# Performance work log

Hardware: AMD Instinct MI355X
Metric: run time of the kernel (lower is better)

## Reference

```python
import jax, jax.numpy as jnp
import numpy as np
from jax import lax

IN_CH = 256
UP = 8
DN = ('NCHW', 'OIHW', 'NCHW')


def setup_inputs() -> dict:
    key = jax.random.key(0)
    ks = jax.random.split(key, 6)
    B, H, W = 8, 96, 96
    flow_lr = jax.random.normal(ks[0], (B, 2, H, W), dtype=jnp.float32)
    feat = jax.random.normal(ks[1], (B, IN_CH, H, W), dtype=jnp.float32)
    w1 = jax.random.normal(ks[2], (IN_CH, IN_CH, 3, 3), dtype=jnp.float32) * 0.02
    b1 = jnp.zeros((IN_CH,), dtype=jnp.float32)
    w2 = jax.random.normal(ks[3], (UP * UP * 9, IN_CH, 1, 1), dtype=jnp.float32) * 0.02
    b2 = jnp.zeros((UP * UP * 9,), dtype=jnp.float32)
    return {"flow_lr": flow_lr, "feat": feat, "w1": w1, "b1": b1, "w2": w2, "b2": b2}


def reference(flow_lr, feat, w1, b1, w2, b2):
    B, _, H, W = flow_lr.shape
    up = UP
    # mask head: 3x3 conv + relu + 1x1 conv
    x = lax.conv_general_dilated(feat, w1, (1, 1), 'SAME', dimension_numbers=DN)
    x = jax.nn.relu(x + b1[None, :, None, None])
    mask = lax.conv_general_dilated(x, w2, (1, 1), 'SAME', dimension_numbers=DN)
    mask = mask + b2[None, :, None, None]
    # channel dim 9*up*up splits as (9, up, up), matching torch .view(B,1,9,up,up,H,W)
    mask = mask.reshape(B, 9, up, up, H, W)
    mask = jax.nn.softmax(mask, axis=1)
    # unfold(flow_lr, 3, padding=1): 9 zero-padded 3x3 shifts, row-major (kh, kw)
    pad = jnp.pad(flow_lr, ((0, 0), (0, 0), (1, 1), (1, 1)))
    flow_unf = jnp.stack(
        [pad[:, :, i:i + H, j:j + W] for i in range(3) for j in range(3)], axis=2
    )  # (B, 2, 9, H, W)
    # convex combination over the 9 neighbors
    up_flow = jnp.einsum('bkpqhw,bckhw->bcpqhw', mask, flow_unf)  # (B,2,up,up,H,W)
    # pixel-shuffle: (B,2,p,q,H,W) -> (B,2,H,p,W,q) -> (B,2,H*up,W*up)
    up_flow = up_flow.transpose(0, 1, 4, 2, 5, 3).reshape(B, 2, H * up, W * up)
    return up_flow * up
```

## Files before the change

kernel.cpp:

```cpp
#include <hip/hip_runtime.h>
#include <hip/hip_bf16.h>
#include <stdint.h>

typedef unsigned short u16;
typedef __bf16 bf16x8 __attribute__((ext_vector_type(8)));
typedef float f32x4 __attribute__((ext_vector_type(4)));

#define MFMA16(a, b, c) __builtin_amdgcn_mfma_f32_16x16x32_bf16((a), (b), (c), 0, 0, 0)

#define GLOAD16(g, l)                                                        \
  __builtin_amdgcn_global_load_lds(                                          \
      (const __attribute__((address_space(1))) void*)(g),                    \
      (__attribute__((address_space(3))) void*)(l), 16, 0, 0)

static __device__ __forceinline__ u16 f2bf(float f) {
  union { float f; uint32_t u; } v;
  v.f = f;
  uint32_t u = v.u;
  return (u16)((u + 0x7FFFu + ((u >> 16) & 1u)) >> 16);
}
static __device__ __forceinline__ float u2f(uint32_t u) {
  union { uint32_t u; float f; } v;
  v.u = u;
  return v.f;
}

#define FEATT_ELEMS (8u * 98u * 98u * 256u)
#define W1T_OFF     FEATT_ELEMS
#define W1T_ELEMS   (256u * 2304u)
#define W2B_OFF     (W1T_OFF + W1T_ELEMS)
#define W2B_ELEMS   (576u * 256u)
#define X_OFF       (W2B_OFF + W2B_ELEMS)

__global__ __launch_bounds__(256) void halo_zero(u16* __restrict__ featT) {
  int tid = blockIdx.x * 256 + threadIdx.x;
  int b = tid / (388 * 32);
  int rem = tid % (388 * 32);
  int pos = rem >> 5, v = rem & 31;
  int h, w;
  if (pos < 98) { h = 0; w = pos; }
  else if (pos < 196) { h = 97; w = pos - 98; }
  else if (pos < 292) { h = pos - 196 + 1; w = 0; }
  else { h = pos - 292 + 1; w = 97; }
  uint4* dst = (uint4*)(featT + (size_t)((b * 98 + h) * 98 + w) * 256 + v * 8);
  *dst = make_uint4(0, 0, 0, 0);
}

__global__ __launch_bounds__(256) void prep_featT(const float* __restrict__ feat,
                                                  u16* __restrict__ featT) {
  const int pt = blockIdx.x, ct = blockIdx.y, b = blockIdx.z;
  const int p0 = pt * 64, c0 = ct * 64;
  __shared__ float tile[64][65];
  const int t = threadIdx.x;
  const int pj = t & 63, ci0 = t >> 6;
#pragma unroll
  for (int r = 0; r < 16; ++r) {
    int ci = r * 4 + ci0;
    tile[ci][pj] = feat[(b * 256 + c0 + ci) * 9216 + p0 + pj];
  }
  __syncthreads();
  const int pl = t >> 2, cc0 = (t & 3) * 16;
  const int pix = p0 + pl;
  const int h = pix / 96, w = pix % 96;
  uint32_t u[8];
#pragma unroll
  for (int i = 0; i < 8; ++i) {
    u16 lo = f2bf(tile[cc0 + 2 * i][pl]);
    u16 hi = f2bf(tile[cc0 + 2 * i + 1][pl]);
    u[i] = (uint32_t)lo | ((uint32_t)hi << 16);
  }
  uint4* dst = (uint4*)(featT + (size_t)((b * 98 + h + 1) * 98 + (w + 1)) * 256 + c0 + cc0);
  dst[0] = make_uint4(u[0], u[1], u[2], u[3]);
  dst[1] = make_uint4(u[4], u[5], u[6], u[7]);
}

__global__ __launch_bounds__(256) void prep_w(const float* __restrict__ w1,
                                              const float* __restrict__ w2,
                                              u16* __restrict__ w1t,
                                              u16* __restrict__ w2b) {
  int i = blockIdx.x * 256 + threadIdx.x;
  if (i < 589824) {
    int oc = i / 2304, r = i % 2304;
    int tap = r >> 8, cin = r & 255;
    w1t[i] = f2bf(w1[(oc * 256 + cin) * 9 + tap]);
  } else {
    int j = i - 589824;
    if (j < 147456) w2b[j] = f2bf(w2[j]);
  }
}

__global__ __launch_bounds__(512, 4) void gemm1(const u16* __restrict__ featT,
                                                const u16* __restrict__ w1t,
                                                const float* __restrict__ b1,
                                                u16* __restrict__ xout) {
  __shared__ __align__(16) u16 sA[128 * 64];
  __shared__ __align__(16) u16 sB[256 * 64];
  __shared__ float sb1[256];

  const int t = threadIdx.x;
  const int wave = t >> 6, lane = t & 63;
  const int mt = blockIdx.x;
  const int b = mt / 72;
  const int ip0 = (mt % 72) * 128;

  if (t < 256) sb1[t] = b1[t];

  const u16* aBase[2];
  const u16* bBase[4];
#pragma unroll
  for (int r = 0; r < 2; ++r) {
    int row = r * 64 + wave * 8 + (lane >> 3);
    int chunk = (lane & 7) ^ (row & 7);
    int ip = ip0 + row;
    int h = ip / 96, w = ip % 96;
    aBase[r] = featT + (size_t)((b * 98 + h + 1) * 98 + (w + 1)) * 256 + chunk * 8;
  }
#pragma unroll
  for (int r = 0; r < 4; ++r) {
    int row = wave * 32 + r * 8 + (lane >> 3);
    int chunk = (lane & 7) ^ (row & 7);
    bBase[r] = w1t + (size_t)row * 2304 + chunk * 8;
  }

  const int wm = wave >> 2, wn = wave & 3;
  int aoffs[4][2], boffs[4][2];
#pragma unroll
  for (int m = 0; m < 4; ++m) {
#pragma unroll
    for (int ki = 0; ki < 2; ++ki) {
      int kc = ki * 4 + (lane >> 4);
      int rowa = wm * 64 + m * 16 + (lane & 15);
      aoffs[m][ki] = rowa * 64 + ((kc ^ (rowa & 7)) * 8);
      int rowb = wn * 64 + m * 16 + (lane & 15);
      boffs[m][ki] = rowb * 64 + ((kc ^ (rowb & 7)) * 8);
    }
  }

  f32x4 acc[4][4];
#pragma unroll
  for (int m = 0; m < 4; ++m)
#pragma unroll
    for (int n = 0; n < 4; ++n) acc[m][n] = f32x4{0.f, 0.f, 0.f, 0.f};

  for (int kt = 0; kt < 36; ++kt) {
    int tap = kt >> 2;
    int dh = tap / 3 - 1, dw = tap % 3 - 1;
    int aoff = (dh * 98 + dw) * 256 + (kt & 3) * 64;
    int boff = kt * 64;
#pragma unroll
    for (int r = 0; r < 2; ++r) GLOAD16(aBase[r] + aoff, &sA[(r * 64 + wave * 8) * 64]);
#pragma unroll
    for (int r = 0; r < 4; ++r) GLOAD16(bBase[r] + boff, &sB[(wave * 32 + r * 8) * 64]);
    __syncthreads();
#pragma unroll
    for (int ki = 0; ki < 2; ++ki) {
      bf16x8 av[4], bv[4];
#pragma unroll
      for (int m = 0; m < 4; ++m) av[m] = *(const bf16x8*)&sA[aoffs[m][ki]];
#pragma unroll
      for (int n = 0; n < 4; ++n) bv[n] = *(const bf16x8*)&sB[boffs[n][ki]];
#pragma unroll
      for (int m = 0; m < 4; ++m)
#pragma unroll
        for (int n = 0; n < 4; ++n) acc[m][n] = MFMA16(av[m], bv[n], acc[m][n]);
    }
    __syncthreads();
  }

  const int pix0g = mt * 128;
#pragma unroll
  for (int m = 0; m < 4; ++m) {
    int pixl = wm * 64 + m * 16 + ((lane >> 4) << 2);
#pragma unroll
    for (int n = 0; n < 4; ++n) {
      int oc = wn * 64 + n * 16 + (lane & 15);
      float bias = sb1[oc];
      f32x4 v = acc[m][n];
#pragma unroll
      for (int j = 0; j < 4; ++j) {
        float val = v[j] + bias;
        val = val > 0.f ? val : 0.f;
        xout[(size_t)(pix0g + pixl + j) * 256 + oc] = f2bf(val);
      }
    }
  }
}

__global__ __launch_bounds__(256) void gemm2t3(const u16* __restrict__ xws,
                                               const u16* __restrict__ w2b,
                                               const float* __restrict__ b2g,
                                               const float* __restrict__ flow,
                                               float* __restrict__ out) {
  __shared__ __align__(16) u16 sW[36864];
  __shared__ uint32_t sFlowP[1152];
  __shared__ float sb2f[576];

  const int t = threadIdx.x;
  const int wave = t >> 6, lane = t & 63;
  const int bid = blockIdx.x;
  const int mt = (bid & 7) * 72 + (bid >> 3);
  const int b = mt / 72;
  const int ipl0 = (mt % 72) * 128;
  const int l15 = lane & 15, kc = lane >> 4;

  auto stageW = [&](int cI) {
#pragma unroll
    for (int pass = 0; pass < 18; ++pass) {
      int c = pass * 256 + t;
      int n = c >> 5, kl = c & 31;
      int kg = kl ^ (n & 31);
      int chan = (n >> 4) * 64 + cI * 16 + (n & 15);
      GLOAD16(w2b + (size_t)chan * 256 + kg * 8, &sW[(pass * 256 + wave * 64) * 8]);
    }
  };
  stageW(0);

  for (int i = t; i < 1152; i += 256) {
    int nf = i >> 7, p = i & 127;
    int ip = ipl0 + p;
    int h = ip / 96, w = ip % 96;
    int hh = h + nf / 3 - 1, ww = w + nf % 3 - 1;
    float vx = 0.f, vy = 0.f;
    if (hh >= 0 && hh < 96 && ww >= 0 && ww < 96) {
      vx = flow[b * 18432 + hh * 96 + ww];
      vy = flow[b * 18432 + 9216 + hh * 96 + ww];
    }
    sFlowP[i] = (uint32_t)f2bf(vx) | ((uint32_t)f2bf(vy) << 16);
  }
  for (int i = t; i < 576; i += 256) sb2f[i] = b2g[i];

  const int pe0 = wave * 32 + l15;
  const int pe1 = pe0 + 16;
  const u16* r0 = &xws[((size_t)mt * 128 + pe0) * 256];
  const u16* r1 = &xws[((size_t)mt * 128 + pe1) * 256];

  __syncthreads();

  uint32_t fpA[9], fpB[9];
#pragma unroll
  for (int nf = 0; nf < 9; ++nf) {
    fpA[nf] = sFlowP[nf * 128 + pe0];
    fpB[nf] = sFlowP[nf * 128 + pe1];
  }
  const int ihA = (ipl0 + pe0) / 96, iwA = (ipl0 + pe0) % 96;
  const int ihB = (ipl0 + pe1) / 96, iwB = (ipl0 + pe1) % 96;
  const size_t obA = ((size_t)(b * 2) * 768 + ihA * 8) * 768 + iwA * 8;
  const size_t obB = ((size_t)(b * 2) * 768 + ihB * 8) * 768 + iwB * 8;

  for (int cI = 0; cI < 4; ++cI) {
    f32x4 accA[9], accB[9];
#pragma unroll
    for (int nf = 0; nf < 9; ++nf) {
      accA[nf] = f32x4{0.f, 0.f, 0.f, 0.f};
      accB[nf] = f32x4{0.f, 0.f, 0.f, 0.f};
    }
    bf16x8 a0A = *(const bf16x8*)&r0[kc * 8];
    bf16x8 a0B = *(const bf16x8*)&r1[kc * 8];
#pragma unroll
    for (int ks = 0; ks < 8; ++ks) {
      bf16x8 a1A, a1B;
      if (ks < 7) {
        a1A = *(const bf16x8*)&r0[((ks + 1) * 4 + kc) * 8];
        a1B = *(const bf16x8*)&r1[((ks + 1) * 4 + kc) * 8];
      }
      int klin = ks * 4 + kc;
      __builtin_amdgcn_s_setprio(1);
#pragma unroll
      for (int nf = 0; nf < 9; ++nf) {
        int n = nf * 16 + l15;
        bf16x8 wv = *(const bf16x8*)&sW[n * 256 + ((klin ^ (n & 31)) * 8)];
        accA[nf] = MFMA16(wv, a0A, accA[nf]);
        accB[nf] = MFMA16(wv, a0B, accB[nf]);
      }
      __builtin_amdgcn_s_setprio(0);
      a0A = a1A;
      a0B = a1B;
    }
    __syncthreads();
    if (cI < 3) stageW(cI + 1);

#pragma unroll
    for (int j = 0; j < 4; ++j) {
      int pql = kc * 4 + j;
      int p = cI * 2 + (pql >> 3), q = pql & 7;
      {
        float v[9], mx = -3.0e38f;
#pragma unroll
        for (int nf = 0; nf < 9; ++nf) {
          v[nf] = accA[nf][j] + sb2f[nf * 64 + cI * 16 + pql];
          mx = fmaxf(mx, v[nf]);
        }
        float ssum = 0.f, fx = 0.f, fy = 0.f;
#pragma unroll
        for (int nf = 0; nf < 9; ++nf) {
          float e = __expf(v[nf] - mx);
          ssum += e;
          fx += e * u2f(fpA[nf] << 16);
          fy += e * u2f(fpA[nf] & 0xFFFF0000u);
        }
        float sc = 8.0f / ssum;
        size_t o0 = obA + (size_t)p * 768 + q;
        out[o0] = fx * sc;
        out[o0 + 589824] = fy * sc;
      }
      {
        float v[9], mx = -3.0e38f;
#pragma unroll
        for (int nf = 0; nf < 9; ++nf) {
          v[nf] = accB[nf][j] + sb2f[nf * 64 + cI * 16 + pql];
          mx = fmaxf(mx, v[nf]);
        }
        float ssum = 0.f, fx = 0.f, fy = 0.f;
#pragma unroll
        for (int nf = 0; nf < 9; ++nf) {
          float e = __expf(v[nf] - mx);
          ssum += e;
          fx += e * u2f(fpB[nf] << 16);
          fy += e * u2f(fpB[nf] & 0xFFFF0000u);
        }
        float sc = 8.0f / ssum;
        size_t o0 = obB + (size_t)p * 768 + q;
        out[o0] = fx * sc;
        out[o0 + 589824] = fy * sc;
      }
    }
    if (cI < 3) __syncthreads();
  }
}

extern "C" void kernel_launch(void* const* d_in, const int* in_sizes, int n_in,
                              void* d_out, int out_size, void* d_ws, size_t ws_size,
                              hipStream_t stream) {
  const float* flow = (const float*)d_in[0];
  const float* feat = (const float*)d_in[1];
  const float* w1 = (const float*)d_in[2];
  const float* b1 = (const float*)d_in[3];
  const float* w2 = (const float*)d_in[4];
  const float* b2 = (const float*)d_in[5];
  float* out = (float*)d_out;
  u16* ws = (u16*)d_ws;
  u16* featT = ws;
  u16* w1t = ws + W1T_OFF;
  u16* w2b = ws + W2B_OFF;
  u16* xws = ws + X_OFF;

  halo_zero<<<388, 256, 0, stream>>>(featT);
  prep_featT<<<dim3(144, 4, 8), 256, 0, stream>>>(feat, featT);
  prep_w<<<2880, 256, 0, stream>>>(w1, w2, w1t, w2b);
  gemm1<<<576, 512, 0, stream>>>(featT, w1t, b1, xws);
  gemm2t3<<<576, 256, 0, stream>>>(xws, w2b, b2, flow, out);
}
```

Baseline: 213.8 us.

## Halve gemm2 weight LDS tile by splitting K into two stages for occupancy

The second GEMM kernel now stages only half of the K dimension (128 of 256) of each weight slice into LDS at a time. This halves the shared weight buffer and adds __launch_bounds__(256,3) so more blocks can be resident per CU. Flow-neighbor values are now read from LDS inside the softmax epilogue instead of being held in registers, which lowers register pressure. In exchange there are twice as many stage/sync rounds, and the weight load for the next half only partially overlaps with compute.

```diff
diff --git a/kernel.cpp b/kernel.cpp
--- a/kernel.cpp
+++ b/kernel.cpp
@@ -186,12 +186,12 @@
   }
 }
 
-__global__ __launch_bounds__(256) void gemm2t3(const u16* __restrict__ xws,
-                                               const u16* __restrict__ w2b,
-                                               const float* __restrict__ b2g,
-                                               const float* __restrict__ flow,
-                                               float* __restrict__ out) {
-  __shared__ __align__(16) u16 sW[36864];
+__global__ __launch_bounds__(256, 3) void gemm2t4(const u16* __restrict__ xws,
+                                                  const u16* __restrict__ w2b,
+                                                  const float* __restrict__ b2g,
+                                                  const float* __restrict__ flow,
+                                                  float* __restrict__ out) {
+  __shared__ __align__(16) u16 sW[18432];
   __shared__ uint32_t sFlowP[1152];
   __shared__ float sb2f[576];
 
@@ -203,17 +203,18 @@
   const int ipl0 = (mt % 72) * 128;
   const int l15 = lane & 15, kc = lane >> 4;
 
-  auto stageW = [&](int cI) {
-#pragma unroll
-    for (int pass = 0; pass < 18; ++pass) {
+  auto stageW = [&](int cI, int kh) {
+#pragma unroll
+    for (int pass = 0; pass < 9; ++pass) {
       int c = pass * 256 + t;
-      int n = c >> 5, kl = c & 31;
-      int kg = kl ^ (n & 31);
+      int n = c >> 4, cl = c & 15;
+      int cg = cl ^ (n & 15);
       int chan = (n >> 4) * 64 + cI * 16 + (n & 15);
-      GLOAD16(w2b + (size_t)chan * 256 + kg * 8, &sW[(pass * 256 + wave * 64) * 8]);
+      GLOAD16(w2b + (size_t)chan * 256 + kh * 128 + cg * 8,
+              &sW[(pass * 256 + wave * 64) * 8]);
     }
   };
-  stageW(0);
+  stageW(0, 0);
 
   for (int i = t; i < 1152; i += 256) {
     int nf = i >> 7, p = i & 127;
@@ -234,97 +235,100 @@
   const u16* r0 = &xws[((size_t)mt * 128 + pe0) * 256];
   const u16* r1 = &xws[((size_t)mt * 128 + pe1) * 256];
 
-  __syncthreads();
-
-  uint32_t fpA[9], fpB[9];
-#pragma unroll
-  for (int nf = 0; nf < 9; ++nf) {
-    fpA[nf] = sFlowP[nf * 128 + pe0];
-    fpB[nf] = sFlowP[nf * 128 + pe1];
-  }
   const int ihA = (ipl0 + pe0) / 96, iwA = (ipl0 + pe0) % 96;
   const int ihB = (ipl0 + pe1) / 96, iwB = (ipl0 + pe1) % 96;
   const size_t obA = ((size_t)(b * 2) * 768 + ihA * 8) * 768 + iwA * 8;
   const size_t obB = ((size_t)(b * 2) * 768 + ihB * 8) * 768 + iwB * 8;
 
+  __syncthreads();
+
+  f32x4 accA[9], accB[9];
   for (int cI = 0; cI < 4; ++cI) {
-    f32x4 accA[9], accB[9];
-#pragma unroll
-    for (int nf = 0; nf < 9; ++nf) {
-      accA[nf] = f32x4{0.f, 0.f, 0.f, 0.f};
-      accB[nf] = f32x4{0.f, 0.f, 0.f, 0.f};
-    }
-    bf16x8 a0A = *(const bf16x8*)&r0[kc * 8];
-    bf16x8 a0B = *(const bf16x8*)&r1[kc * 8];
-#pragma unroll
-    for (int ks = 0; ks < 8; ++ks) {
-      bf16x8 a1A, a1B;
-      if (ks < 7) {
-        a1A = *(const bf16x8*)&r0[((ks + 1) * 4 + kc) * 8];
-        a1B = *(const bf16x8*)&r1[((ks + 1) * 4 + kc) * 8];
+#pragma unroll
+    for (int kh = 0; kh < 2; ++kh) {
+      if (kh == 0) {
+#pragma unroll
+        for (int nf = 0; nf < 9; ++nf) {
+          accA[nf] = f32x4{0.f, 0.f, 0.f, 0.f};
+          accB[nf] = f32x4{0.f, 0.f, 0.f, 0.f};
+        }
       }
-      int klin = ks * 4 + kc;
+      bf16x8 a0A = *(const bf16x8*)&r0[(kh * 16 + kc) * 8];
+      bf16x8 a0B = *(const bf16x8*)&r1[(kh * 16 + kc) * 8];
       __builtin_amdgcn_s_setprio(1);
 #pragma unroll
-      for (int nf = 0; nf < 9; ++nf) {
-        int n = nf * 16 + l15;
-        bf16x8 wv = *(const bf16x8*)&sW[n * 256 + ((klin ^ (n & 31)) * 8)];
-        accA[nf] = MFMA16(wv, a0A, accA[nf]);
-        accB[nf] = MFMA16(wv, a0B, accB[nf]);
+      for (int ks = 0; ks < 4; ++ks) {
+        bf16x8 a1A, a1B;
+        if (ks < 3) {
+          a1A = *(const bf16x8*)&r0[(kh * 16 + (ks + 1) * 4 + kc) * 8];
+          a1B = *(const bf16x8*)&r1[(kh * 16 + (ks + 1) * 4 + kc) * 8];
+        }
+        int kcc = ks * 4 + kc;
+#pragma unroll
+        for (int nf = 0; nf < 9; ++nf) {
+          int n = nf * 16 + l15;
+          bf16x8 wv = *(const bf16x8*)&sW[n * 128 + ((kcc ^ (n & 15)) * 8)];
+          accA[nf] = MFMA16(wv, a0A, accA[nf]);
+          accB[nf] = MFMA16(wv, a0B, accB[nf]);
+        }
+        a0A = a1A;
+        a0B = a1B;
       }
       __builtin_amdgcn_s_setprio(0);
-      a0A = a1A;
-      a0B = a1B;
-    }
-    __syncthreads();
-    if (cI < 3) stageW(cI + 1);
-
-#pragma unroll
-    for (int j = 0; j < 4; ++j) {
-      int pql = kc * 4 + j;
-      int p = cI * 2 + (pql >> 3), q = pql & 7;
-      {
-        float v[9], mx = -3.0e38f;
-#pragma unroll
-        for (int nf = 0; nf < 9; ++nf) {
-          v[nf] = accA[nf][j] + sb2f[nf * 64 + cI * 16 + pql];
-          mx = fmaxf(mx, v[nf]);
+      __syncthreads();
+      if (!(cI == 3 && kh == 1)) stageW(cI + (kh == 1 ? 1 : 0), kh ^ 1);
+
+      if (kh == 1) {
+#pragma unroll
+        for (int j = 0; j < 4; ++j) {
+          int pql = kc * 4 + j;
+          int p = cI * 2 + (pql >> 3), q = pql & 7;
+          {
+            float v[9], mx = -3.0e38f;
+#pragma unroll
+            for (int nf = 0; nf < 9; ++nf) {
+              v[nf] = accA[nf][j] + sb2f[nf * 64 + cI * 16 + pql];
+              mx = fmaxf(mx, v[nf]);
+            }
+            float ssum = 0.f, fx = 0.f, fy = 0.f;
+#pragma unroll
+            for (int nf = 0; nf < 9; ++nf) {
+              float e = __expf(v[nf] - mx);
+              ssum += e;
+              uint32_t fp = sFlowP[nf * 128 + pe0];
+              fx += e * u2f(fp << 16);
+              fy += e * u2f(fp & 0xFFFF0000u);
+            }
+            float sc = 8.0f / ssum;
+            size_t o0 = obA + (size_t)p * 768 + q;
+            out[o0] = fx * sc;
+            out[o0 + 589824] = fy * sc;
+          }
+          {
+            float v[9], mx = -3.0e38f;
+#pragma unroll
+            for (int nf = 0; nf < 9; ++nf) {
+              v[nf] = accB[nf][j] + sb2f[nf * 64 + cI * 16 + pql];
+              mx = fmaxf(mx, v[nf]);
+            }
+            float ssum = 0.f, fx = 0.f, fy = 0.f;
+#pragma unroll
+            for (int nf = 0; nf < 9; ++nf) {
+              float e = __expf(v[nf] - mx);
+              ssum += e;
+              uint32_t fp = sFlowP[nf * 128 + pe1];
+              fx += e * u2f(fp << 16);
+              fy += e * u2f(fp & 0xFFFF0000u);
+            }
+            float sc = 8.0f / ssum;
+            size_t o0 = obB + (size_t)p * 768 + q;
+            out[o0] = fx * sc;
+            out[o0 + 589824] = fy * sc;
+          }
         }
-        float ssum = 0.f, fx = 0.f, fy = 0.f;
-#pragma unroll
-        for (int nf = 0; nf < 9; ++nf) {
-          float e = __expf(v[nf] - mx);
-          ssum += e;
-          fx += e * u2f(fpA[nf] << 16);
-          fy += e * u2f(fpA[nf] & 0xFFFF0000u);
-        }
-        float sc = 8.0f / ssum;
-        size_t o0 = obA + (size_t)p * 768 + q;
-        out[o0] = fx * sc;
-        out[o0 + 589824] = fy * sc;
       }
-      {
-        float v[9], mx = -3.0e38f;
-#pragma unroll
-        for (int nf = 0; nf < 9; ++nf) {
-          v[nf] = accB[nf][j] + sb2f[nf * 64 + cI * 16 + pql];
-          mx = fmaxf(mx, v[nf]);
-        }
-        float ssum = 0.f, fx = 0.f, fy = 0.f;
-#pragma unroll
-        for (int nf = 0; nf < 9; ++nf) {
-          float e = __expf(v[nf] - mx);
-          ssum += e;
-          fx += e * u2f(fpB[nf] << 16);
-          fy += e * u2f(fpB[nf] & 0xFFFF0000u);
-        }
-        float sc = 8.0f / ssum;
-        size_t o0 = obB + (size_t)p * 768 + q;
-        out[o0] = fx * sc;
-        out[o0 + 589824] = fy * sc;
-      }
-    }
-    if (cI < 3) __syncthreads();
+      __syncthreads();
+    }
   }
 }
 
@@ -348,5 +352,5 @@
   prep_featT<<<dim3(144, 4, 8), 256, 0, stream>>>(feat, featT);
   prep_w<<<2880, 256, 0, stream>>>(w1, w2, w1t, w2b);
   gemm1<<<576, 512, 0, stream>>>(featT, w1t, b1, xws);
-  gemm2t3<<<576, 256, 0, stream>>>(xws, w2b, b2, flow, out);
-}
+  gemm2t4<<<576, 256, 0, stream>>>(xws, w2b, b2, flow, out);
+}
```

New measurement: 241.1 us. 12.8% more time.
